# Performance work log

Hardware: AMD Instinct MI355X
Metric: run time of the kernel (lower is better)

The kernel has to match this reference:

```python
import jax, jax.numpy as jnp
import numpy as np

# Enformer/Borzoi-style MHA with relative positional bias
B, T, C = 2, 1536, 1536          # batch, seq bins, input channels
H, K, V = 8, 64, 192             # heads, key_size, value_size
F = 32                           # num_position_features (borzoi, asymmetric: 2 * 16 basis)


def setup_inputs() -> dict:
    key = jax.random.key(0)
    ks = jax.random.split(key, 9)
    he = lambda fan_in: (2.0 / fan_in) ** 0.5  # he_normal scale
    return {
        "x": jax.random.normal(ks[0], (B, T, C), jnp.float32),
        "Wq": jax.random.normal(ks[1], (C, H * K), jnp.float32) * he(C),
        "Wk": jax.random.normal(ks[2], (C, H * K), jnp.float32) * he(C),
        "Wv": jax.random.normal(ks[3], (C, H * V), jnp.float32) * he(C),
        "Wr": jax.random.normal(ks[4], (F, H * K), jnp.float32) * he(F),
        "r_w_bias": jax.random.normal(ks[5], (1, H, 1, K), jnp.float32) * 0.02,
        "r_r_bias": jax.random.normal(ks[6], (1, H, 1, K), jnp.float32) * 0.02,
        "Wo": jax.random.normal(ks[7], (H * V, H * V), jnp.float32) * he(H * V),
        "bo": jnp.zeros((H * V,), jnp.float32),
    }


def positional_features(positions):
    """Borzoi central-mask basis, absolute=True, asymmetric -> [L, F]."""
    nb = F // 2
    pow_rate = np.exp(np.log(T + 1) / nb).astype(np.float32)
    center_widths = pow_rate ** jnp.arange(1, nb + 1, dtype=jnp.float32) - 1.0  # [nb]
    sign = jnp.sign(positions)
    abs_pos = jnp.abs(positions)
    emb = (center_widths[None, :] > abs_pos[:, None]).astype(jnp.float32)  # [L, nb]
    return jnp.concatenate([emb, sign[:, None] * emb], axis=-1)  # [L, 2*nb]


def relative_shift(x):
    """[B,H,T,2T-1] -> [B,H,T,T] relative-shift trick (pad, reshape, slice)."""
    b, h, t, l = x.shape
    x = jnp.pad(x, ((0, 0), (0, 0), (0, 0), (1, 0)))      # [b,h,t,l+1]
    x = x.reshape(b, h, l + 1, t)[:, :, 1:, :]             # [b,h,l,t]
    x = x.reshape(b, h, t, l)
    return x[..., :t]


def reference(x, Wq, Wk, Wv, Wr, r_w_bias, r_r_bias, Wo, bo):
    q = (x @ Wq).reshape(B, T, H, K).transpose(0, 2, 1, 3)   # [B,H,T,K]
    k = (x @ Wk).reshape(B, T, H, K).transpose(0, 2, 1, 3)
    v = (x @ Wv).reshape(B, T, H, V).transpose(0, 2, 1, 3)   # [B,H,T,V]
    q = q * (K ** -0.5)  # scaling=True

    distances = jnp.arange(-T + 1, T, dtype=jnp.float32)     # [2T-1]
    pe = positional_features(distances)                       # [2T-1, F]
    rk = (pe @ Wr).reshape(2 * T - 1, H, K)                   # [2T-1, H, K]

    content_logits = jnp.einsum('bhtk,bhsk->bhts', q + r_w_bias, k)   # [B,H,T,T]
    rel_logits = jnp.einsum('bhtk,rhk->bhtr', q + r_r_bias, rk)       # [B,H,T,2T-1]
    logits = content_logits + relative_shift(rel_logits)

    weights = jax.nn.softmax(logits, axis=-1)
    out = jnp.einsum('bhts,bhsv->bhtv', weights, v)          # [B,H,T,V]
    out = out.transpose(0, 2, 1, 3).reshape(B, T, H * V)     # [B,T,H*V]
    return out @ Wo + bo
```

## Files before the change

kernel.cpp:

```cpp
#include <hip/hip_runtime.h>
#include <hip/hip_bf16.h>

typedef __hip_bfloat16 bf16;
typedef unsigned short ushort;
typedef unsigned int uint;
typedef __attribute__((ext_vector_type(8))) short short8;
typedef __attribute__((ext_vector_type(4))) float f32x4;

#define Bsz 2
#define Tn  1536
#define Cn  1536
#define Hn  8
#define Kn  64
#define Vn  192

__device__ __forceinline__ ushort f2bs(float f) {
  union { bf16 h; ushort u; } cv;
  cv.h = __float2bfloat16(f);
  return cv.u;
}
__device__ __forceinline__ float bs2f(ushort u) {
  union { float f; uint v; } cv; cv.v = ((uint)u) << 16; return cv.f;
}

__device__ __forceinline__ void gld_lds16(const ushort* g, ushort* l) {
  __builtin_amdgcn_global_load_lds(
      (const __attribute__((address_space(1))) uint*)g,
      (__attribute__((address_space(3))) uint*)l, 16, 0, 0);
}

#define DPP_MAXSTEP(x, ctrl)                                                  \
  do {                                                                        \
    union { float f; int i; } a_, b_;                                         \
    a_.f = (x);                                                               \
    b_.i = __builtin_amdgcn_update_dpp(a_.i, a_.i, (ctrl), 0xf, 0xf, true);   \
    (x) = fmaxf((x), b_.f);                                                   \
  } while (0)

__global__ __launch_bounds__(256) void prep(
    const float* __restrict__ x,  const float* __restrict__ Wq,
    const float* __restrict__ Wk, const float* __restrict__ Wv,
    const float* __restrict__ Wo, const float* __restrict__ Wr,
    ushort* __restrict__ xb, ushort* __restrict__ Wt,
    ushort* __restrict__ Wot, ushort* __restrict__ rkdb,
    unsigned char* __restrict__ lutb) {
  const int z = blockIdx.z;
  if (z < 4) {
    if (z < 2 && blockIdx.x >= 16) return;
    const float* in = (z == 0) ? Wq : (z == 1) ? Wk : (z == 2) ? Wv : Wo;
    ushort* out = (z == 0) ? Wt : (z == 1) ? Wt + 512 * 1536
                : (z == 2) ? Wt + 1024 * 1536 : Wot;
    const int Cc = (z < 2) ? 512 : 1536;
    __shared__ float tile[32][33];
    const int bx = blockIdx.x * 32;
    const int by = blockIdx.y * 32;
    const int tx = threadIdx.x & 31, ty = threadIdx.x >> 5;
#pragma unroll
    for (int i = 0; i < 32; i += 8)
      tile[ty + i][tx] = in[(size_t)(by + ty + i) * Cc + bx + tx];
    __syncthreads();
#pragma unroll
    for (int i = 0; i < 32; i += 8)
      out[(size_t)(bx + ty + i) * 1536 + by + tx] = f2bs(tile[tx][ty + i]);
  } else if (z == 4) {
    const int n4 = 3072 * 1536 / 4;
    for (int i = (blockIdx.y * 48 + blockIdx.x) * 256 + threadIdx.x; i < n4;
         i += 2304 * 256) {
      float4 v = ((const float4*)x)[i];
      uint2 o;
      o.x = (uint)f2bs(v.x) | ((uint)f2bs(v.y) << 16);
      o.y = (uint)f2bs(v.z) | ((uint)f2bs(v.w) << 16);
      ((uint2*)xb)[i] = o;
    }
  } else {
    const int base = (blockIdx.y * 48 + blockIdx.x) * 256 + threadIdx.x;
    if (base < 8 * 40 * 64) {
      const int h = base / 2560, rem = base % 2560, u = rem >> 6, k = rem & 63;
      float acc = 0.f;
      if (u < 33) {
        const float sg = (u == 32) ? 0.f : (u < 16 ? 1.f : -1.f);
        const int c = (u == 32) ? 16 : (u < 16 ? u + 1 : u - 15);
#pragma unroll
        for (int i = 0; i < 16; i++)
          if (i >= 16 - c)
            acc += Wr[i * 512 + h * 64 + k] + sg * Wr[(16 + i) * 512 + h * 64 + k];
      }
      rkdb[h * 2560 + u * 64 + k] = f2bs(acc);
    } else if (base < 8 * 40 * 64 + 3072) {
      const int idx = base - 8 * 40 * 64;
      const int d = idx - 1535;
      const float ad = fabsf((float)d);
      int c = 0;
#pragma unroll
      for (int i = 0; i < 16; i++) {
        double cw = exp(log((double)(Tn + 1)) * (double)(i + 1) / 16.0) - 1.0;
        if ((float)cw > ad) c++;
      }
      lutb[idx] = (unsigned char)((d == 0) ? 32 : (d > 0 ? c - 1 : 15 + c));
    }
  }
}

__global__ __launch_bounds__(256) void gemm_qkv(
    const ushort* __restrict__ xb, const ushort* __restrict__ Wt,
    ushort* __restrict__ qb, ushort* __restrict__ kb, ushort* __restrict__ vtb) {
  __shared__ ushort Al[128 * 32];
  __shared__ ushort Bl[128 * 32];
  const int tid = threadIdx.x;
  const int w = tid >> 6, lane = tid & 63, quad = lane >> 4, ln = lane & 15;
  const int bm = blockIdx.y * 128, bn = blockIdx.x * 128;
  const int wm = (w & 1) * 64, wn = (w >> 1) * 64;
  f32x4 acc[4][4];
#pragma unroll
  for (int i = 0; i < 4; i++)
#pragma unroll
    for (int j = 0; j < 4; j++) acc[i][j] = (f32x4){0.f, 0.f, 0.f, 0.f};

  for (int k0 = 0; k0 < 1536; k0 += 32) {
    __syncthreads();
#pragma unroll
    for (int st = 0; st < 2; st++) {
      int idx = tid + st * 256;
      int row = idx >> 2, col = (idx & 3) * 8;
      gld_lds16(xb + (size_t)(bm + row) * 1536 + k0 + col, Al + idx * 8);
      gld_lds16(Wt + (size_t)(bn + row) * 1536 + k0 + col, Bl + idx * 8);
    }
    __syncthreads();
    short8 af[4], bfr[4];
#pragma unroll
    for (int t = 0; t < 4; t++) {
      af[t]  = *(const short8*)(Al + (wm + t * 16 + ln) * 32 + quad * 8);
      bfr[t] = *(const short8*)(Bl + (wn + t * 16 + ln) * 32 + quad * 8);
    }
#pragma unroll
    for (int mt = 0; mt < 4; mt++)
#pragma unroll
      for (int nt = 0; nt < 4; nt++)
        acc[mt][nt] = __builtin_amdgcn_mfma_f32_16x16x32_bf16(
            af[mt], bfr[nt], acc[mt][nt], 0, 0, 0);
  }

  if (bn < 512) {
#pragma unroll
    for (int mt = 0; mt < 4; mt++)
#pragma unroll
      for (int nt = 0; nt < 4; nt++)
#pragma unroll
        for (int r = 0; r < 4; r++) {
          int m = bm + wm + mt * 16 + quad * 4 + r;
          int n = bn + wn + nt * 16 + ln;
          qb[(size_t)m * 512 + n] = f2bs(acc[mt][nt][r] * 0.125f);
        }
  } else if (bn < 1024) {
#pragma unroll
    for (int mt = 0; mt < 4; mt++)
#pragma unroll
      for (int nt = 0; nt < 4; nt++)
#pragma unroll
        for (int r = 0; r < 4; r++) {
          int m = bm + wm + mt * 16 + quad * 4 + r;
          int n = bn - 512 + wn + nt * 16 + ln;
          kb[(size_t)m * 512 + n] = f2bs(acc[mt][nt][r]);
        }
  } else {
#pragma unroll
    for (int mt = 0; mt < 4; mt++)
#pragma unroll
      for (int nt = 0; nt < 4; nt++) {
        int vcol = bn - 1024 + wn + nt * 16 + ln;
        int m0 = bm + wm + mt * 16 + quad * 4;
        uint2 val;
        val.x = (uint)f2bs(acc[mt][nt][0]) | ((uint)f2bs(acc[mt][nt][1]) << 16);
        val.y = (uint)f2bs(acc[mt][nt][2]) | ((uint)f2bs(acc[mt][nt][3]) << 16);
        *(uint2*)(vtb + (size_t)vcol * 3072 + m0) = val;
      }
  }
}

__global__ __launch_bounds__(256) void gemm_out(
    const ushort* __restrict__ att, const ushort* __restrict__ Wot,
    const float* __restrict__ bo, float* __restrict__ out) {
  __shared__ ushort Al[128 * 32];
  __shared__ ushort Bl[128 * 32];
  const int tid = threadIdx.x;
  const int w = tid >> 6, lane = tid & 63, quad = lane >> 4, ln = lane & 15;
  const int bm = blockIdx.y * 128, bn = blockIdx.x * 128;
  const int wm = (w & 1) * 64, wn = (w >> 1) * 64;
  f32x4 acc[4][4];
#pragma unroll
  for (int i = 0; i < 4; i++)
#pragma unroll
    for (int j = 0; j < 4; j++) acc[i][j] = (f32x4){0.f, 0.f, 0.f, 0.f};

  for (int k0 = 0; k0 < 1536; k0 += 32) {
    __syncthreads();
#pragma unroll
    for (int st = 0; st < 2; st++) {
      int idx = tid + st * 256;
      int row = idx >> 2, col = (idx & 3) * 8;
      gld_lds16(att + (size_t)(bm + row) * 1536 + k0 + col, Al + idx * 8);
      gld_lds16(Wot + (size_t)(bn + row) * 1536 + k0 + col, Bl + idx * 8);
    }
    __syncthreads();
    short8 af[4], bfr[4];
#pragma unroll
    for (int t = 0; t < 4; t++) {
      af[t]  = *(const short8*)(Al + (wm + t * 16 + ln) * 32 + quad * 8);
      bfr[t] = *(const short8*)(Bl + (wn + t * 16 + ln) * 32 + quad * 8);
    }
#pragma unroll
    for (int mt = 0; mt < 4; mt++)
#pragma unroll
      for (int nt = 0; nt < 4; nt++)
        acc[mt][nt] = __builtin_amdgcn_mfma_f32_16x16x32_bf16(
            af[mt], bfr[nt], acc[mt][nt], 0, 0, 0);
  }
#pragma unroll
  for (int mt = 0; mt < 4; mt++)
#pragma unroll
    for (int nt = 0; nt < 4; nt++)
#pragma unroll
      for (int r = 0; r < 4; r++) {
        int m = bm + wm + mt * 16 + quad * 4 + r;
        int n = bn + wn + nt * 16 + ln;
        out[(size_t)m * 1536 + n] = acc[mt][nt][r] + bo[n];
      }
}

__global__ __launch_bounds__(256, 3) void attn_mfma(
    const ushort* __restrict__ qb, const ushort* __restrict__ kb,
    const ushort* __restrict__ vtb, const ushort* __restrict__ rkdb,
    const unsigned char* __restrict__ lutb,
    const float* __restrict__ rwb, const float* __restrict__ rrb,
    ushort* __restrict__ op0, ushort* __restrict__ op1,
    float2* __restrict__ mlb) {
  __shared__ __align__(16) char smem[50176];
  ushort* Kl = (ushort*)smem;
  ushort* Vl = (ushort*)(smem + 8192);
  ushort* Dl = (ushort*)(smem + 32768);
  unsigned char* Ll = (unsigned char*)(smem + 37888);

  const int L  = blockIdx.x + 24 * blockIdx.y + 192 * blockIdx.z;
  const int h  = L & 7;
  const int g  = L >> 3;
  const int bsk = g / 24;
  const int b  = bsk >> 1;
  const int sk = bsk & 1;
  const int t0 = (g - bsk * 24) * 64;
  const int bT = b * Tn;
  const int tid = threadIdx.x;
  const int w = tid >> 6, lane = tid & 63, quad = lane >> 4, ln = lane & 15;

  ushort* Pp = (ushort*)(smem + 40960 + w * 2304);

  const int lr  = lane >> 3;
  const int lcx = (lane & 7) ^ lr;

  {
    const int s0 = sk * 768;
#pragma unroll
    for (int i = 0; i < 2; i++) {
      int kc = w * 2 + i, sr = kc * 8 + lr;
      gld_lds16(kb + (size_t)(bT + s0 + sr) * 512 + h * 64 + lcx * 8,
                (ushort*)(smem + kc * 1024) + lane * 8);
    }
#pragma unroll
    for (int i = 0; i < 6; i++) {
      int kc = w * 6 + i, vr = kc * 8 + lr;
      gld_lds16(vtb + (size_t)(h * 192 + vr) * 3072 + bT + s0 + lcx * 8,
                (ushort*)(smem + 8192 + kc * 1024) + lane * 8);
    }
    if (w < 3)
      gld_lds16((const ushort*)(lutb + w * 1024) + lane * 8,
                (ushort*)(smem + 37888 + w * 1024) + lane * 8);
  }

  short8 qw8[2], qr8[2];
  {
    const ushort* qrow = qb + (size_t)(bT + t0 + 16 * w + ln) * 512 + h * 64;
#pragma unroll
    for (int ks = 0; ks < 2; ks++) {
      int k0 = quad * 8 + ks * 32;
#pragma unroll
      for (int e = 0; e < 8; e++) {
        float qv = bs2f(qrow[k0 + e]);
        qw8[ks][e] = (short)f2bs(qv + rwb[h * 64 + k0 + e]);
        qr8[ks][e] = (short)f2bs(qv + rrb[h * 64 + k0 + e]);
      }
    }
  }

  {
    f32x4 Dacc[3];
#pragma unroll
    for (int ut = 0; ut < 3; ut++) {
      Dacc[ut] = (f32x4){0.f, 0.f, 0.f, 0.f};
#pragma unroll
      for (int ks = 0; ks < 2; ks++) {
        int urow = 16 * ut + ln; urow = urow > 39 ? 39 : urow;
        short8 bfr = *(const short8*)(rkdb + h * 2560 + urow * 64 + quad * 8 + ks * 32);
        Dacc[ut] = __builtin_amdgcn_mfma_f32_16x16x32_bf16(qr8[ks], bfr, Dacc[ut], 0, 0, 0);
      }
    }
    const int trow = 16 * w + 4 * quad;
#pragma unroll
    for (int ut = 0; ut < 2; ut++)
#pragma unroll
      for (int r = 0; r < 4; r++)
        Dl[(trow + r) * 40 + 16 * ut + ln] = f2bs(Dacc[ut][r]);
    if (ln == 0) {
#pragma unroll
      for (int r = 0; r < 4; r++)
        Dl[(trow + r) * 40 + 32] = f2bs(Dacc[2][r]);
    }
  }

  f32x4 Oacc[12];
  f32x4 Lacc = (f32x4){0.f, 0.f, 0.f, 0.f};
  float m_i[4];
#pragma unroll
  for (int vt = 0; vt < 12; vt++) Oacc[vt] = (f32x4){0.f, 0.f, 0.f, 0.f};
#pragma unroll
  for (int r = 0; r < 4; r++) m_i[r] = -1e30f;

  short8 ones8;
#pragma unroll
  for (int e = 0; e < 8; e++) ones8[e] = (short)0x3F80;

  __syncthreads();

  const int ibase = sk * 768 - t0 - 16 * w - 4 * quad + ln + 1535;
  const int tl0 = 16 * w + 4 * quad;

  for (int ch = 0; ch < 12; ch++) {
    float dval[4][4];
#pragma unroll
    for (int ct = 0; ct < 4; ct++)
#pragma unroll
      for (int r = 0; r < 4; r++) {
        int idx = ibase + 64 * ch + 16 * ct - r;
        dval[ct][r] = bs2f(Dl[(tl0 + r) * 40 + Ll[idx]]);
      }

    f32x4 Sacc[4];
    __builtin_amdgcn_s_setprio(1);
#pragma unroll
    for (int ct = 0; ct < 4; ct++) {
      Sacc[ct] = (f32x4){0.f, 0.f, 0.f, 0.f};
#pragma unroll
      for (int ks = 0; ks < 2; ks++) {
        short8 bfr = *(const short8*)(
            Kl + (16 * ct + ln) * 64 + ((quad + 4 * ks) ^ (ln & 7)) * 8);
        Sacc[ct] = __builtin_amdgcn_mfma_f32_16x16x32_bf16(qw8[ks], bfr, Sacc[ct], 0, 0, 0);
      }
    }
    __builtin_amdgcn_s_setprio(0);

    float pS[4][4];
#pragma unroll
    for (int ct = 0; ct < 4; ct++)
#pragma unroll
      for (int r = 0; r < 4; r++)
        pS[ct][r] = Sacc[ct][r] + dval[ct][r];

    float alpha[4];
#pragma unroll
    for (int r = 0; r < 4; r++) {
      float mx = fmaxf(fmaxf(pS[0][r], pS[1][r]), fmaxf(pS[2][r], pS[3][r]));
      DPP_MAXSTEP(mx, 0xB1);
      DPP_MAXSTEP(mx, 0x4E);
      DPP_MAXSTEP(mx, 0x124);
      DPP_MAXSTEP(mx, 0x128);
      float mnew = fmaxf(m_i[r], mx);
      alpha[r] = __expf(m_i[r] - mnew);
      m_i[r] = mnew;
#pragma unroll
      for (int ct = 0; ct < 4; ct++)
        pS[ct][r] = __expf(pS[ct][r] - mnew);
    }
#pragma unroll
    for (int vt = 0; vt < 12; vt++)
#pragma unroll
      for (int r = 0; r < 4; r++) Oacc[vt][r] *= alpha[r];
#pragma unroll
    for (int r = 0; r < 4; r++) Lacc[r] *= alpha[r];
#pragma unroll
    for (int ct = 0; ct < 4; ct++)
#pragma unroll
      for (int r = 0; r < 4; r++)
        Pp[(4 * quad + r) * 72 + 16 * ct + ln] = f2bs(pS[ct][r]);
    __asm__ volatile("s_waitcnt lgkmcnt(0)" ::: "memory");
    short8 afr[2];
#pragma unroll
    for (int ks = 0; ks < 2; ks++)
      afr[ks] = *(const short8*)(Pp + ln * 72 + quad * 8 + ks * 32);

    __syncthreads();

    if (ch < 11) {
      const int s0n = sk * 768 + ch * 64 + 64;
#pragma unroll
      for (int i = 0; i < 2; i++) {
        int kc = w * 2 + i, sr = kc * 8 + lr;
        gld_lds16(kb + (size_t)(bT + s0n + sr) * 512 + h * 64 + lcx * 8,
                  (ushort*)(smem + kc * 1024) + lane * 8);
      }
    }

    __builtin_amdgcn_s_setprio(1);
    Lacc = __builtin_amdgcn_mfma_f32_16x16x32_bf16(afr[0], ones8, Lacc, 0, 0, 0);
    Lacc = __builtin_amdgcn_mfma_f32_16x16x32_bf16(afr[1], ones8, Lacc, 0, 0, 0);
#pragma unroll
    for (int vt = 0; vt < 12; vt++) {
#pragma unroll
      for (int ks = 0; ks < 2; ks++) {
        short8 bfr = *(const short8*)(
            Vl + (16 * vt + ln) * 64 + ((quad + 4 * ks) ^ (ln & 7)) * 8);
        Oacc[vt] = __builtin_amdgcn_mfma_f32_16x16x32_bf16(afr[ks], bfr, Oacc[vt], 0, 0, 0);
      }
    }
    __builtin_amdgcn_s_setprio(0);

    __syncthreads();

    if (ch < 11) {
      const int s0n = sk * 768 + ch * 64 + 64;
#pragma unroll
      for (int i = 0; i < 6; i++) {
        int kc = w * 6 + i, vr = kc * 8 + lr;
        gld_lds16(vtb + (size_t)(h * 192 + vr) * 3072 + bT + s0n + lcx * 8,
                  (ushort*)(smem + 8192 + kc * 1024) + lane * 8);
      }
    }
  }

  ushort* op = sk ? op1 : op0;
  float inv[4];
#pragma unroll
  for (int r = 0; r < 4; r++) inv[r] = 1.f / Lacc[r];
#pragma unroll
  for (int vt = 0; vt < 12; vt++)
#pragma unroll
    for (int r = 0; r < 4; r++) {
      int t = t0 + 16 * w + 4 * quad + r;
      op[(size_t)(bT + t) * 1536 + h * 192 + 16 * vt + ln] = f2bs(Oacc[vt][r] * inv[r]);
    }
  if (ln == 0) {
#pragma unroll
    for (int r = 0; r < 4; r++) {
      int t = t0 + 16 * w + 4 * quad + r;
      float2 v; v.x = m_i[r]; v.y = Lacc[r];
      mlb[((sk * 2 + b) * 8 + h) * 1536 + t] = v;
    }
  }
}

__global__ __launch_bounds__(256) void attn_combine(
    const ushort* __restrict__ op0, const ushort* __restrict__ op1,
    const float2* __restrict__ mlb, ushort* __restrict__ att) {
  int g = blockIdx.x * 256 + threadIdx.x;
  int row = g / 384;
  int c4 = (g - row * 384) * 4;
  int b = row >= 1536;
  int t = row - b * 1536;
  int h = c4 / 192;
  float2 ml0 = mlb[((0 + b) * 8 + h) * 1536 + t];
  float2 ml1 = mlb[((2 + b) * 8 + h) * 1536 + t];
  float M = fmaxf(ml0.x, ml1.x);
  float w0 = __expf(ml0.x - M) * ml0.y;
  float w1 = __expf(ml1.x - M) * ml1.y;
  float inv = 1.f / (w0 + w1);
  w0 *= inv; w1 *= inv;
  size_t off = (size_t)row * 1536 + c4;
  uint2 a = *(const uint2*)(op0 + off);
  uint2 c = *(const uint2*)(op1 + off);
  uint2 o;
  float r0 = w0 * bs2f((ushort)(a.x & 0xffff)) + w1 * bs2f((ushort)(c.x & 0xffff));
  float r1 = w0 * bs2f((ushort)(a.x >> 16))    + w1 * bs2f((ushort)(c.x >> 16));
  float r2 = w0 * bs2f((ushort)(a.y & 0xffff)) + w1 * bs2f((ushort)(c.y & 0xffff));
  float r3 = w0 * bs2f((ushort)(a.y >> 16))    + w1 * bs2f((ushort)(c.y >> 16));
  o.x = (uint)f2bs(r0) | ((uint)f2bs(r1) << 16);
  o.y = (uint)f2bs(r2) | ((uint)f2bs(r3) << 16);
  *(uint2*)(att + off) = o;
}

extern "C" void kernel_launch(void* const* d_in, const int* in_sizes, int n_in,
                              void* d_out, int out_size, void* d_ws, size_t ws_size,
                              hipStream_t stream) {
  const float* x   = (const float*)d_in[0];
  const float* Wq  = (const float*)d_in[1];
  const float* Wk  = (const float*)d_in[2];
  const float* Wv  = (const float*)d_in[3];
  const float* Wr  = (const float*)d_in[4];
  const float* rwb = (const float*)d_in[5];
  const float* rrb = (const float*)d_in[6];
  const float* Wo  = (const float*)d_in[7];
  const float* bo  = (const float*)d_in[8];
  float* out = (float*)d_out;

  char* ws = (char*)d_ws;
  ushort* xb  = (ushort*)ws;
  ushort* op1 = (ushort*)ws;
  ushort* att = (ushort*)ws;
  ushort* Wot = (ushort*)(ws + 9437184);
  ushort* Wt  = (ushort*)(ws + 14155776);
  ushort* op0 = (ushort*)(ws + 14155776);
  ushort* qb  = (ushort*)(ws + 23592960);
  ushort* kb  = (ushort*)(ws + 26738688);
  ushort* vtb = (ushort*)(ws + 29884416);
  unsigned char* lutb = (unsigned char*)(ws + 41287680);
  ushort* rkdb = (ushort*)(ws + 41290752);
  float2* mlb = (float2*)(ws + 42467328);

  prep<<<dim3(48, 48, 6), dim3(256), 0, stream>>>(
      x, Wq, Wk, Wv, Wo, Wr, xb, Wt, Wot, rkdb, lutb);
  gemm_qkv<<<dim3(20, 24), dim3(256), 0, stream>>>(xb, Wt, qb, kb, vtb);
  attn_mfma<<<dim3(24, 8, 4), dim3(256), 0, stream>>>(
      qb, kb, vtb, rkdb, lutb, rwb, rrb, op0, op1, mlb);
  attn_combine<<<dim3(4608), dim3(256), 0, stream>>>(op0, op1, mlb, att);
  gemm_out<<<dim3(12, 24), dim3(256), 0, stream>>>(att, Wot, bo, out);
}
```

Before: 224.3 us.

## Add lazy softmax rescaling and grouped tile ordering for GEMMs

The flash-attention loop now updates the running max, and rescales the output and sum accumulators, only when some row's new block max exceeds the stored max by more than 8. Otherwise it exponentiates against the stale max, which skips the 48-element accumulator multiply on most iterations. Both GEMM kernels also remap block indices into a grouped order, aiming for better L2 reuse of A and B tiles across co-resident workgroups. The lazy rescale lets exponentials grow up to e^8, which bf16 P and fp32 accumulators should tolerate, and adds a wave-wide vote branch.

```diff
diff --git a/kernel.cpp b/kernel.cpp
--- a/kernel.cpp
+++ b/kernel.cpp
@@ -108,7 +108,9 @@
   __shared__ ushort Bl[128 * 32];
   const int tid = threadIdx.x;
   const int w = tid >> 6, lane = tid & 63, quad = lane >> 4, ln = lane & 15;
-  const int bm = blockIdx.y * 128, bn = blockIdx.x * 128;
+  const int Lb = blockIdx.x + 20 * blockIdx.y;
+  const int wg = (Lb & 7) * 60 + (Lb >> 3);
+  const int bm = (wg % 24) * 128, bn = (wg / 24) * 128;
   const int wm = (w & 1) * 64, wn = (w >> 1) * 64;
   f32x4 acc[4][4];
 #pragma unroll
@@ -184,7 +186,9 @@
   __shared__ ushort Bl[128 * 32];
   const int tid = threadIdx.x;
   const int w = tid >> 6, lane = tid & 63, quad = lane >> 4, ln = lane & 15;
-  const int bm = blockIdx.y * 128, bn = blockIdx.x * 128;
+  const int Lb = blockIdx.x + 12 * blockIdx.y;
+  const int wg = (Lb & 7) * 36 + (Lb >> 3);
+  const int bm = (wg % 24) * 128, bn = (wg / 24) * 128;
   const int wm = (w & 1) * 64, wn = (w >> 1) * 64;
   f32x4 acc[4][4];
 #pragma unroll
@@ -363,27 +367,34 @@
       for (int r = 0; r < 4; r++)
         pS[ct][r] = Sacc[ct][r] + dval[ct][r];
 
-    float alpha[4];
+    float mx[4];
 #pragma unroll
     for (int r = 0; r < 4; r++) {
-      float mx = fmaxf(fmaxf(pS[0][r], pS[1][r]), fmaxf(pS[2][r], pS[3][r]));
-      DPP_MAXSTEP(mx, 0xB1);
-      DPP_MAXSTEP(mx, 0x4E);
-      DPP_MAXSTEP(mx, 0x124);
-      DPP_MAXSTEP(mx, 0x128);
-      float mnew = fmaxf(m_i[r], mx);
-      alpha[r] = __expf(m_i[r] - mnew);
-      m_i[r] = mnew;
-#pragma unroll
-      for (int ct = 0; ct < 4; ct++)
-        pS[ct][r] = __expf(pS[ct][r] - mnew);
-    }
-#pragma unroll
-    for (int vt = 0; vt < 12; vt++)
-#pragma unroll
-      for (int r = 0; r < 4; r++) Oacc[vt][r] *= alpha[r];
-#pragma unroll
-    for (int r = 0; r < 4; r++) Lacc[r] *= alpha[r];
+      float m2 = fmaxf(fmaxf(pS[0][r], pS[1][r]), fmaxf(pS[2][r], pS[3][r]));
+      DPP_MAXSTEP(m2, 0xB1);
+      DPP_MAXSTEP(m2, 0x4E);
+      DPP_MAXSTEP(m2, 0x124);
+      DPP_MAXSTEP(m2, 0x128);
+      mx[r] = m2;
+    }
+    int need = (mx[0] > m_i[0] + 8.f) | (mx[1] > m_i[1] + 8.f) |
+               (mx[2] > m_i[2] + 8.f) | (mx[3] > m_i[3] + 8.f);
+    if (__any(need)) {
+#pragma unroll
+      for (int r = 0; r < 4; r++) {
+        float mnew = fmaxf(m_i[r], mx[r]);
+        float alpha = __expf(m_i[r] - mnew);
+        m_i[r] = mnew;
+        Lacc[r] *= alpha;
+#pragma unroll
+        for (int vt = 0; vt < 12; vt++) Oacc[vt][r] *= alpha;
+      }
+    }
+#pragma unroll
+    for (int ct = 0; ct < 4; ct++)
+#pragma unroll
+      for (int r = 0; r < 4; r++)
+        pS[ct][r] = __expf(pS[ct][r] - m_i[r]);
 #pragma unroll
     for (int ct = 0; ct < 4; ct++)
 #pragma unroll
```

Measured after the change: 221.2 us. No clear change (-1.4%).
